# Performance work log

Measured on AMD Instinct MI355X. Metric: run time of the kernel, lower is better.

The kernel has to match this reference:

```python
import jax, jax.numpy as jnp
import numpy as np

N_EMBD = 768
N_HEAD = 12

def setup_inputs() -> dict:
    key = jax.random.key(0)
    ks = jax.random.split(key, 10)
    B, T, C = 2, 2048, N_EMBD
    s = 1.0 / np.sqrt(C)
    x = jax.random.normal(ks[0], (B, T, C), dtype=jnp.float32)
    attn_mask = jnp.ones((B, 1, T, T), dtype=jnp.float32)
    Wq = jax.random.normal(ks[1], (C, C), dtype=jnp.float32) * s
    bq = jax.random.normal(ks[2], (C,), dtype=jnp.float32) * 0.01
    Wk = jax.random.normal(ks[3], (C, C), dtype=jnp.float32) * s
    bk = jax.random.normal(ks[4], (C,), dtype=jnp.float32) * 0.01
    Wv = jax.random.normal(ks[5], (C, C), dtype=jnp.float32) * s
    bv = jax.random.normal(ks[6], (C,), dtype=jnp.float32) * 0.01
    Wp = jax.random.normal(ks[7], (C, C), dtype=jnp.float32) * s
    bp = jax.random.normal(ks[8], (C,), dtype=jnp.float32) * 0.01
    return {"x": x, "attn_mask": attn_mask, "Wq": Wq, "bq": bq, "Wk": Wk, "bk": bk,
            "Wv": Wv, "bv": bv, "Wp": Wp, "bp": bp}

def reference(x, attn_mask, Wq, bq, Wk, bk, Wv, bv, Wp, bp):
    B, T, C = x.shape
    H = N_HEAD
    hd = C // H
    # Linear layers (torch nn.Linear: y = x @ W.T + b)
    q = (x @ Wq.T + bq).reshape(B, T, H, hd).transpose(0, 2, 1, 3)  # [B,H,T,hd]
    k = (x @ Wk.T + bk).reshape(B, T, H, hd).transpose(0, 2, 1, 3)
    v = (x @ Wv.T + bv).reshape(B, T, H, hd).transpose(0, 2, 1, 3)
    att = jnp.einsum('bhqd,bhkd->bhqk', q, k) / jnp.sqrt(jnp.float32(hd))  # [B,H,T,T]
    causal = jnp.tril(jnp.ones((T, T), dtype=jnp.bool_))[None, None]       # [1,1,T,T]
    combined = causal & (attn_mask > 0)                                    # broadcast to [B,H,T,T]
    att = jnp.where(combined, att, -jnp.inf)
    att = jax.nn.softmax(att, axis=-1)
    y = jnp.einsum('bhqk,bhkd->bhqd', att, v)                              # [B,H,T,hd]
    y = y.transpose(0, 2, 1, 3).reshape(B, T, C)
    return y @ Wp.T + bp
```

## Files before the change

### kernel.cpp

```cpp
#include <hip/hip_runtime.h>
#include <hip/hip_bf16.h>
#include <cstdint>
#include <cstddef>

#define B_   2
#define H_   12
#define T_   2048
#define C_   768
#define HD_  64
#define M_   4096
#define NW_  (T_/64)
#define NPAIR 2

typedef __attribute__((ext_vector_type(8))) short bf16x8;
typedef __attribute__((ext_vector_type(4))) float fx4;
typedef __attribute__((ext_vector_type(16))) float f32x16;
typedef unsigned short u16;
typedef unsigned int   u32;
typedef unsigned long long u64;

static __device__ __forceinline__ u16 f2bf(float f){
    union { float f; unsigned int i; } c; c.f = f;
    unsigned int x = c.i;
    return (u16)((x + 0x7fffu + ((x >> 16) & 1u)) >> 16);
}

static __device__ __forceinline__ u32 pack_bf2(float a, float b){
    union { __hip_bfloat162 h; u32 u; } cv;
    cv.h = __float22bfloat162_rn(make_float2(a, b));
    return cv.u;
}

#define PREP_XBLK (M_ * C_ / 4 / 256)
#define PREP_WBLK (4 * C_ * C_ / 4 / 256)
#define PREP_MBLK (B_ * T_ * NW_ / 4)
__global__ void prep(const float* __restrict__ x,
                     const float* __restrict__ wq, const float* __restrict__ wk,
                     const float* __restrict__ wv, const float* __restrict__ wp,
                     const float* __restrict__ mask,
                     u16* __restrict__ xb, u16* __restrict__ wqkv, u64* __restrict__ bits)
{
    int bx = blockIdx.x;
    if (bx < PREP_XBLK){
        int i = bx * 256 + threadIdx.x;
        float4 v = ((const float4*)x)[i];
        ushort4 o;
        o.x = f2bf(v.x); o.y = f2bf(v.y); o.z = f2bf(v.z); o.w = f2bf(v.w);
        ((ushort4*)xb)[i] = o;
    } else if (bx < PREP_XBLK + PREP_WBLK){
        int i = (bx - PREP_XBLK) * 256 + threadIdx.x;
        int wsel = i / (C_ * C_ / 4);
        int wi   = i % (C_ * C_ / 4);
        const float* src = (wsel == 0) ? wq : (wsel == 1) ? wk : (wsel == 2) ? wv : wp;
        float4 v = ((const float4*)src)[wi];
        ushort4 o;
        o.x = f2bf(v.x); o.y = f2bf(v.y); o.z = f2bf(v.z); o.w = f2bf(v.w);
        ((ushort4*)wqkv)[i] = o;
    } else {
        int wid  = (bx - PREP_XBLK - PREP_WBLK) * 4 + (threadIdx.x >> 6);
        int lane = threadIdx.x & 63;
        float v = mask[(size_t)wid * 64 + lane];
        u64 m = __ballot(v > 0.0f);
        if (lane == 0) bits[wid] = m;
    }
}

__launch_bounds__(256, 2)
__global__ void gemm_qkv(const u16* __restrict__ xb, const u16* __restrict__ wqkv,
                         const float* __restrict__ bq, const float* __restrict__ bk,
                         const float* __restrict__ bv,
                         u16* __restrict__ qo, u16* __restrict__ ko, u16* __restrict__ vto)
{
    const int tid  = threadIdx.x;
    const int lane = tid & 63, wave = tid >> 6;
    const int l15 = lane & 15, lg = lane >> 4;
    int flat = blockIdx.x + 6 * (blockIdx.y + 32 * blockIdx.z);
    int swz  = (flat & 7) * 72 + (flat >> 3);
    const int n0 = (swz % 6) * 128;
    const int m0 = ((swz / 6) % 32) * 128;
    const int z  = swz / 192;
    const u16* wb     = wqkv + (size_t)z * C_ * C_;
    const float* bias = (z == 0) ? bq : (z == 1 ? bk : bv);
    const float oscl  = (z == 0) ? 0.1803368801111601f : 1.0f;

    __shared__ __align__(16) u16 lds_a[128 * 64];
    __shared__ __align__(16) u16 lds_b[128 * 64];

    fx4 acc[4][4];
    #pragma unroll
    for (int i = 0; i < 4; i++)
        #pragma unroll
        for (int j = 0; j < 4; j++) acc[i][j] = (fx4)0.0f;

    const int wm = (wave >> 1) * 64, wn = (wave & 1) * 64;
    const int sx = l15 & 7;

    for (int kt = 0; kt < C_ / 64; ++kt){
        const int k0 = kt * 64;
        #pragma unroll
        for (int c = 0; c < 4; ++c){
            int unit = c * 256 + tid;
            int row = unit >> 3, col = unit & 7;
            int gcol = (col ^ (row & 7)) * 8;
            const u16* ga = xb + (size_t)(m0 + row) * C_ + k0 + gcol;
            __builtin_amdgcn_global_load_lds((const __attribute__((address_space(1))) void*)ga,
                (__attribute__((address_space(3))) void*)(lds_a + (c * 256 + wave * 64) * 8), 16, 0, 0);
            const u16* gb = wb + (size_t)(n0 + row) * C_ + k0 + gcol;
            __builtin_amdgcn_global_load_lds((const __attribute__((address_space(1))) void*)gb,
                (__attribute__((address_space(3))) void*)(lds_b + (c * 256 + wave * 64) * 8), 16, 0, 0);
        }
        __syncthreads();
        #pragma unroll
        for (int ks = 0; ks < 2; ++ks){
            bf16x8 af[4], bfr[4];
            #pragma unroll
            for (int i = 0; i < 4; i++){
                af[i]  = *(const bf16x8*)&lds_a[(wm + i * 16 + l15) * 64 + (((4 * ks + lg) ^ sx) * 8)];
                bfr[i] = *(const bf16x8*)&lds_b[(wn + i * 16 + l15) * 64 + (((4 * ks + lg) ^ sx) * 8)];
            }
            #pragma unroll
            for (int i = 0; i < 4; i++)
                #pragma unroll
                for (int j = 0; j < 4; j++)
                    acc[i][j] = __builtin_amdgcn_mfma_f32_16x16x32_bf16(af[i], bfr[j], acc[i][j], 0, 0, 0);
        }
        __syncthreads();
    }

    #pragma unroll
    for (int i = 0; i < 4; i++){
        #pragma unroll
        for (int j = 0; j < 4; j++){
            #pragma unroll
            for (int r = 0; r < 4; r++){
                int m = m0 + wm + i * 16 + lg * 4 + r;
                int n = n0 + wn + j * 16 + l15;
                float v = (acc[i][j][r] + bias[n]) * oscl;
                u16 o = f2bf(v);
                int b = m >> 11, t = m & (T_ - 1);
                int h = n >> 6, d = n & 63;
                if (z == 2){
                    vto[(size_t)((b * H_ + h) * HD_ + d) * T_ + t] = o;
                } else {
                    u16* dst = (z == 0) ? qo : ko;
                    dst[(size_t)((b * H_ + h) * T_ + t) * HD_ + d] = o;
                }
            }
        }
    }
}

__launch_bounds__(256, 2)
__global__ void gemm_proj(const u16* __restrict__ yb, const u16* __restrict__ wp,
                          const float* __restrict__ bp, float* __restrict__ out)
{
    const int tid  = threadIdx.x;
    const int lane = tid & 63, wave = tid >> 6;
    const int l15 = lane & 15, lg = lane >> 4;
    int flat = blockIdx.x + 6 * blockIdx.y;
    int swz  = (flat & 7) * 24 + (flat >> 3);
    const int n0 = (swz % 6) * 128;
    const int m0 = (swz / 6) * 128;

    __shared__ __align__(16) u16 lds_a[128 * 64];
    __shared__ __align__(16) u16 lds_b[128 * 64];

    fx4 acc[4][4];
    #pragma unroll
    for (int i = 0; i < 4; i++)
        #pragma unroll
        for (int j = 0; j < 4; j++) acc[i][j] = (fx4)0.0f;

    const int wm = (wave >> 1) * 64, wn = (wave & 1) * 64;
    const int sx = l15 & 7;

    for (int kt = 0; kt < C_ / 64; ++kt){
        const int k0 = kt * 64;
        #pragma unroll
        for (int c = 0; c < 4; ++c){
            int unit = c * 256 + tid;
            int row = unit >> 3, col = unit & 7;
            int gcol = (col ^ (row & 7)) * 8;
            const u16* ga = yb + (size_t)(m0 + row) * C_ + k0 + gcol;
            __builtin_amdgcn_global_load_lds((const __attribute__((address_space(1))) void*)ga,
                (__attribute__((address_space(3))) void*)(lds_a + (c * 256 + wave * 64) * 8), 16, 0, 0);
            const u16* gb = wp + (size_t)(n0 + row) * C_ + k0 + gcol;
            __builtin_amdgcn_global_load_lds((const __attribute__((address_space(1))) void*)gb,
                (__attribute__((address_space(3))) void*)(lds_b + (c * 256 + wave * 64) * 8), 16, 0, 0);
        }
        __syncthreads();
        #pragma unroll
        for (int ks = 0; ks < 2; ++ks){
            bf16x8 af[4], bfr[4];
            #pragma unroll
            for (int i = 0; i < 4; i++){
                af[i]  = *(const bf16x8*)&lds_a[(wm + i * 16 + l15) * 64 + (((4 * ks + lg) ^ sx) * 8)];
                bfr[i] = *(const bf16x8*)&lds_b[(wn + i * 16 + l15) * 64 + (((4 * ks + lg) ^ sx) * 8)];
            }
            #pragma unroll
            for (int i = 0; i < 4; i++)
                #pragma unroll
                for (int j = 0; j < 4; j++)
                    acc[i][j] = __builtin_amdgcn_mfma_f32_16x16x32_bf16(af[i], bfr[j], acc[i][j], 0, 0, 0);
        }
        __syncthreads();
    }

    #pragma unroll
    for (int i = 0; i < 4; i++)
        #pragma unroll
        for (int j = 0; j < 4; j++)
            #pragma unroll
            for (int r = 0; r < 4; r++){
                int m = m0 + wm + i * 16 + lg * 4 + r;
                int n = n0 + wn + j * 16 + l15;
                out[(size_t)m * C_ + n] = acc[i][j][r] + bp[n];
            }
}

__launch_bounds__(256)
__global__ void attn(const u16* __restrict__ q, const u16* __restrict__ kmat,
                     const u16* __restrict__ vt, const u64* __restrict__ bits,
                     u16* __restrict__ y)
{
    const int tid = threadIdx.x;
    const int pr  = tid >> 7;
    const int ptid = tid & 127;
    const int w2  = (tid >> 6) & 1;
    const int lane = tid & 63;
    const int l31 = lane & 31, hi = lane >> 5;

    int flat = blockIdx.x;
    const int bh = (flat & 7) * 3 + ((flat >> 3) % 3);
    const int qt = 31 - (flat >> 3) / 3;
    const int b = bh / H_, h = bh % H_;
    const int qw0 = qt * 64 + 32 * w2;

    extern __shared__ __align__(16) u16 smem[];
    u16* lds_k = smem + (size_t)pr * 8192;
    u16* lds_v = lds_k + 4096;
    float* lds_ml = (float*)smem;

    const size_t bhoff = (size_t)bh * T_ * HD_;
    const u16* kb_ = kmat + bhoff;
    const u16* vb_ = vt + bhoff;

    bf16x8 qf[4];
    {
        const u16* qrow = q + bhoff + (size_t)(qw0 + l31) * HD_ + hi * 8;
        #pragma unroll
        for (int dc = 0; dc < 4; dc++)
            qf[dc] = *(const bf16x8*)(qrow + dc * 16);
    }

    f32x16 o0 = (f32x16)0.0f, o1 = (f32x16)0.0f;
    float m_l = -1e30f, l_l = 0.0f;

    const int nkt = qt + 1;
    const int nit = (nkt + NPAIR - 1) / NPAIR;
    const int qg  = qw0 + l31;
    const u64* brow = bits + (size_t)(b * T_ + qg) * NW_;

    for (int it = 0; it < nit; ++it){
        const int kt = it * NPAIR + pr;
        const bool valid = kt < nkt;
        const int kbase = kt * 64;

        if (it > 0) __syncthreads();
        if (valid){
            #pragma unroll
            for (int i = 0; i < 4; i++){
                int u = i * 128 + ptid;
                int row = u >> 3, col = u & 7;
                int gcol = (col ^ (row & 7)) * 8;
                __builtin_amdgcn_global_load_lds(
                    (const __attribute__((address_space(1))) void*)(kb_ + (size_t)(kbase + row) * HD_ + gcol),
                    (__attribute__((address_space(3))) void*)(lds_k + u * 8), 16, 0, 0);
                __builtin_amdgcn_global_load_lds(
                    (const __attribute__((address_space(1))) void*)(vb_ + (size_t)row * T_ + kbase + gcol),
                    (__attribute__((address_space(3))) void*)(lds_v + u * 8), 16, 0, 0);
            }
        }
        __syncthreads();

        if (valid){
            f32x16 s0 = (f32x16)0.0f, s1 = (f32x16)0.0f;
            #pragma unroll
            for (int dc = 0; dc < 4; dc++){
                bf16x8 kf0 = *(const bf16x8*)&lds_k[(l31     ) * 64 + (((2 * dc + hi) ^ (l31 & 7)) * 8)];
                bf16x8 kf1 = *(const bf16x8*)&lds_k[(l31 + 32) * 64 + (((2 * dc + hi) ^ (l31 & 7)) * 8)];
                s0 = __builtin_amdgcn_mfma_f32_32x32x16_bf16(kf0, qf[dc], s0, 0, 0, 0);
                s1 = __builtin_amdgcn_mfma_f32_32x32x16_bf16(kf1, qf[dc], s1, 0, 0, 0);
            }

            u64 raw = brow[kt];
            int sh = qg - kbase;
            u64 vis = sh < 0 ? 0ull : (sh >= 63 ? ~0ull : ((2ull << sh) - 1ull));
            u64 masked = raw & vis;
            if (!__all(masked == ~0ull)){
                u32 mk0 = (u32)(masked >> (4 * hi));
                u32 mk1 = (u32)(masked >> (32 + 4 * hi));
                #pragma unroll
                for (int r = 0; r < 16; r++){
                    int bpos = (r & 3) + 8 * (r >> 2);
                    s0[r] = ((mk0 >> bpos) & 1u) ? s0[r] : -1e30f;
                    s1[r] = ((mk1 >> bpos) & 1u) ? s1[r] : -1e30f;
                }
            }

            float mx = -1e30f;
            #pragma unroll
            for (int r = 0; r < 16; r++){ mx = fmaxf(mx, s0[r]); mx = fmaxf(mx, s1[r]); }
            mx = fmaxf(mx, __shfl_xor(mx, 32, 64));

            if (!__all(mx <= m_l + 10.0f)){
                float mnew = fmaxf(m_l, mx);
                float al = __builtin_amdgcn_exp2f(m_l - mnew);
                m_l = mnew;
                l_l *= al;
                #pragma unroll
                for (int r = 0; r < 16; r++){
                    int ql = (r & 3) + 8 * (r >> 2) + 4 * hi;
                    float a_r = __shfl(al, ql, 64);
                    o0[r] *= a_r; o1[r] *= a_r;
                }
            }

            float rs = 0.0f;
            bf16x8 pa[2][2];
            #pragma unroll
            for (int kb = 0; kb < 2; kb++){
                u32 P[8];
                #pragma unroll
                for (int g = 0; g < 8; g++){
                    float pe0 = __builtin_amdgcn_exp2f((kb ? s1[2*g]   : s0[2*g])   - m_l);
                    float pe1 = __builtin_amdgcn_exp2f((kb ? s1[2*g+1] : s0[2*g+1]) - m_l);
                    rs += pe0 + pe1;
                    P[g] = pack_bf2(pe0, pe1);
                }
                asm volatile("v_permlane32_swap_b32 %0, %1" : "+v"(P[0]), "+v"(P[2]));
                asm volatile("v_permlane32_swap_b32 %0, %1" : "+v"(P[1]), "+v"(P[3]));
                asm volatile("v_permlane32_swap_b32 %0, %1" : "+v"(P[4]), "+v"(P[6]));
                asm volatile("v_permlane32_swap_b32 %0, %1" : "+v"(P[5]), "+v"(P[7]));
                union { u32 uw[4]; bf16x8 v; } u0, u1;
                u0.uw[0]=P[0]; u0.uw[1]=P[1]; u0.uw[2]=P[2]; u0.uw[3]=P[3];
                u1.uw[0]=P[4]; u1.uw[1]=P[5]; u1.uw[2]=P[6]; u1.uw[3]=P[7];
                pa[kb][0] = u0.v; pa[kb][1] = u1.v;
            }
            rs += __shfl_xor(rs, 32, 64);
            l_l += rs;

            #pragma unroll
            for (int kb = 0; kb < 2; kb++)
                #pragma unroll
                for (int ks = 0; ks < 2; ks++){
                    int gidx = 4 * kb + 2 * ks + hi;
                    bf16x8 vf0 = *(const bf16x8*)&lds_v[(l31     ) * 64 + ((gidx ^ (l31 & 7)) * 8)];
                    bf16x8 vf1 = *(const bf16x8*)&lds_v[(l31 + 32) * 64 + ((gidx ^ (l31 & 7)) * 8)];
                    o0 = __builtin_amdgcn_mfma_f32_32x32x16_bf16(pa[kb][ks], vf0, o0, 0, 0, 0);
                    o1 = __builtin_amdgcn_mfma_f32_32x32x16_bf16(pa[kb][ks], vf1, o1, 0, 0, 0);
                }
        }
    }

    __syncthreads();
    {
        const int qrow = w2 * 32 + l31;
        if (hi == 0){
            lds_ml[(pr * 2 + 0) * 64 + qrow] = m_l;
            lds_ml[(pr * 2 + 1) * 64 + qrow] = l_l;
        }
        if (pr != 0){
            float* Od = (float*)(smem + (size_t)pr * 8192);
            #pragma unroll
            for (int r = 0; r < 16; r++){
                int ql = (r & 3) + 8 * (r >> 2) + 4 * hi;
                int row = w2 * 32 + ql;
                Od[row * 64 + l31]      = o0[r];
                Od[row * 64 + 32 + l31] = o1[r];
            }
        }
    }
    __syncthreads();

    if (pr == 0){
        const int qrow = w2 * 32 + l31;
        float mvals[NPAIR], lvals[NPAIR];
        mvals[0] = m_l; lvals[0] = l_l;
        #pragma unroll
        for (int p = 1; p < NPAIR; p++){
            mvals[p] = lds_ml[(p * 2 + 0) * 64 + qrow];
            lvals[p] = lds_ml[(p * 2 + 1) * 64 + qrow];
        }
        float mm = mvals[0];
        #pragma unroll
        for (int p = 1; p < NPAIR; p++) mm = fmaxf(mm, mvals[p]);
        float a[NPAIR], ltot = 0.0f;
        #pragma unroll
        for (int p = 0; p < NPAIR; p++){
            a[p] = __builtin_amdgcn_exp2f(mvals[p] - mm);
            ltot += lvals[p] * a[p];
        }
        float inv = 1.0f / ltot;

        #pragma unroll
        for (int r = 0; r < 16; r++){
            int ql = (r & 3) + 8 * (r >> 2) + 4 * hi;
            int row = w2 * 32 + ql;
            float a0r = __shfl(a[0], ql, 64);
            float v0 = o0[r] * a0r;
            float v1 = o1[r] * a0r;
            #pragma unroll
            for (int p = 1; p < NPAIR; p++){
                float apr = __shfl(a[p], ql, 64);
                const float* Od = (const float*)(smem + (size_t)p * 8192);
                v0 += Od[row * 64 + l31]      * apr;
                v1 += Od[row * 64 + 32 + l31] * apr;
            }
            float ivr = __shfl(inv, ql, 64);
            int trow = qt * 64 + row;
            u16* yr = y + (size_t)(b * T_ + trow) * C_ + h * HD_;
            yr[l31]      = f2bf(v0 * ivr);
            yr[32 + l31] = f2bf(v1 * ivr);
        }
    }
}

extern "C" void kernel_launch(void* const* d_in, const int* in_sizes, int n_in,
                              void* d_out, int out_size, void* d_ws, size_t ws_size,
                              hipStream_t stream)
{
    const float* x    = (const float*)d_in[0];
    const float* mask = (const float*)d_in[1];
    const float* Wq   = (const float*)d_in[2];
    const float* bq   = (const float*)d_in[3];
    const float* Wk   = (const float*)d_in[4];
    const float* bk   = (const float*)d_in[5];
    const float* Wv   = (const float*)d_in[6];
    const float* bv   = (const float*)d_in[7];
    const float* Wp   = (const float*)d_in[8];
    const float* bp   = (const float*)d_in[9];
    float* out = (float*)d_out;

    char* p = (char*)d_ws;
    u16* xb   = (u16*)p; p += (size_t)M_ * C_ * 2;
    u16* wqkv = (u16*)p; p += (size_t)4 * C_ * C_ * 2;
    u16* qo   = (u16*)p; p += (size_t)M_ * C_ * 2;
    u16* ko   = (u16*)p; p += (size_t)M_ * C_ * 2;
    u16* vto  = (u16*)p; p += (size_t)M_ * C_ * 2;
    u16* yb   = (u16*)p; p += (size_t)M_ * C_ * 2;
    u64* bits = (u64*)p; p += (size_t)B_ * T_ * NW_ * 8;

    prep<<<dim3(PREP_XBLK + PREP_WBLK + PREP_MBLK), 256, 0, stream>>>(
        x, Wq, Wk, Wv, Wp, mask, xb, wqkv, bits);

    gemm_qkv<<<dim3(C_ / 128, M_ / 128, 3), 256, 0, stream>>>(
        xb, wqkv, bq, bk, bv, qo, ko, vto);

    attn<<<dim3((T_ / 64) * B_ * H_), 256, NPAIR * 8192 * sizeof(u16), stream>>>(
        qo, ko, vto, bits, yb);

    gemm_proj<<<dim3(C_ / 128, M_ / 128), 256, 0, stream>>>(yb, wqkv + (size_t)3 * C_ * C_, bp, out);
}
```

Baseline: 113.8 us.

## Double-buffer LDS tiles in QKV and projection GEMMs to overlap loads with MFMA

Both GEMM kernels now use two LDS buffers per operand. The next K-tile is issued through global_load_lds into the alternate buffer while MFMAs run on the current one, so global-load latency overlaps with compute and one barrier per iteration is dropped. In exchange LDS use doubles to 64KB per block and the min-blocks-per-SM launch bound is removed, which can lower occupancy. The single barrier after compute must also cover completion of the async LDS writes, and the compiler's vmcnt handling decides whether real overlap happens.

```diff
diff --git a/kernel.cpp b/kernel.cpp
--- a/kernel.cpp
+++ b/kernel.cpp
@@ -65,7 +65,7 @@
     }
 }
 
-__launch_bounds__(256, 2)
+__launch_bounds__(256)
 __global__ void gemm_qkv(const u16* __restrict__ xb, const u16* __restrict__ wqkv,
                          const float* __restrict__ bq, const float* __restrict__ bk,
                          const float* __restrict__ bv,
@@ -83,8 +83,8 @@
     const float* bias = (z == 0) ? bq : (z == 1 ? bk : bv);
     const float oscl  = (z == 0) ? 0.1803368801111601f : 1.0f;
 
-    __shared__ __align__(16) u16 lds_a[128 * 64];
-    __shared__ __align__(16) u16 lds_b[128 * 64];
+    __shared__ __align__(16) u16 lds_a[2][128 * 64];
+    __shared__ __align__(16) u16 lds_b[2][128 * 64];
 
     fx4 acc[4][4];
     #pragma unroll
@@ -94,8 +94,9 @@
 
     const int wm = (wave >> 1) * 64, wn = (wave & 1) * 64;
     const int sx = l15 & 7;
-
-    for (int kt = 0; kt < C_ / 64; ++kt){
+    const int NT = C_ / 64;
+
+    auto stage = [&](int buf, int kt){
         const int k0 = kt * 64;
         #pragma unroll
         for (int c = 0; c < 4; ++c){
@@ -104,19 +105,25 @@
             int gcol = (col ^ (row & 7)) * 8;
             const u16* ga = xb + (size_t)(m0 + row) * C_ + k0 + gcol;
             __builtin_amdgcn_global_load_lds((const __attribute__((address_space(1))) void*)ga,
-                (__attribute__((address_space(3))) void*)(lds_a + (c * 256 + wave * 64) * 8), 16, 0, 0);
+                (__attribute__((address_space(3))) void*)(&lds_a[buf][(c * 256 + wave * 64) * 8]), 16, 0, 0);
             const u16* gb = wb + (size_t)(n0 + row) * C_ + k0 + gcol;
             __builtin_amdgcn_global_load_lds((const __attribute__((address_space(1))) void*)gb,
-                (__attribute__((address_space(3))) void*)(lds_b + (c * 256 + wave * 64) * 8), 16, 0, 0);
-        }
-        __syncthreads();
+                (__attribute__((address_space(3))) void*)(&lds_b[buf][(c * 256 + wave * 64) * 8]), 16, 0, 0);
+        }
+    };
+
+    stage(0, 0);
+    __syncthreads();
+    int cur = 0;
+    for (int kt = 0; kt < NT; ++kt){
+        if (kt + 1 < NT) stage(cur ^ 1, kt + 1);
         #pragma unroll
         for (int ks = 0; ks < 2; ++ks){
             bf16x8 af[4], bfr[4];
             #pragma unroll
             for (int i = 0; i < 4; i++){
-                af[i]  = *(const bf16x8*)&lds_a[(wm + i * 16 + l15) * 64 + (((4 * ks + lg) ^ sx) * 8)];
-                bfr[i] = *(const bf16x8*)&lds_b[(wn + i * 16 + l15) * 64 + (((4 * ks + lg) ^ sx) * 8)];
+                af[i]  = *(const bf16x8*)&lds_a[cur][(wm + i * 16 + l15) * 64 + (((4 * ks + lg) ^ sx) * 8)];
+                bfr[i] = *(const bf16x8*)&lds_b[cur][(wn + i * 16 + l15) * 64 + (((4 * ks + lg) ^ sx) * 8)];
             }
             #pragma unroll
             for (int i = 0; i < 4; i++)
@@ -125,6 +132,7 @@
                     acc[i][j] = __builtin_amdgcn_mfma_f32_16x16x32_bf16(af[i], bfr[j], acc[i][j], 0, 0, 0);
         }
         __syncthreads();
+        cur ^= 1;
     }
 
     #pragma unroll
@@ -150,7 +158,7 @@
     }
 }
 
-__launch_bounds__(256, 2)
+__launch_bounds__(256)
 __global__ void gemm_proj(const u16* __restrict__ yb, const u16* __restrict__ wp,
                           const float* __restrict__ bp, float* __restrict__ out)
 {
@@ -162,8 +170,8 @@
     const int n0 = (swz % 6) * 128;
     const int m0 = (swz / 6) * 128;
 
-    __shared__ __align__(16) u16 lds_a[128 * 64];
-    __shared__ __align__(16) u16 lds_b[128 * 64];
+    __shared__ __align__(16) u16 lds_a[2][128 * 64];
+    __shared__ __align__(16) u16 lds_b[2][128 * 64];
 
     fx4 acc[4][4];
     #pragma unroll
@@ -173,8 +181,9 @@
 
     const int wm = (wave >> 1) * 64, wn = (wave & 1) * 64;
     const int sx = l15 & 7;
-
-    for (int kt = 0; kt < C_ / 64; ++kt){
+    const int NT = C_ / 64;
+
+    auto stage = [&](int buf, int kt){
         const int k0 = kt * 64;
         #pragma unroll
         for (int c = 0; c < 4; ++c){
@@ -183,19 +192,25 @@
             int gcol = (col ^ (row & 7)) * 8;
             const u16* ga = yb + (size_t)(m0 + row) * C_ + k0 + gcol;
             __builtin_amdgcn_global_load_lds((const __attribute__((address_space(1))) void*)ga,
-                (__attribute__((address_space(3))) void*)(lds_a + (c * 256 + wave * 64) * 8), 16, 0, 0);
+                (__attribute__((address_space(3))) void*)(&lds_a[buf][(c * 256 + wave * 64) * 8]), 16, 0, 0);
             const u16* gb = wp + (size_t)(n0 + row) * C_ + k0 + gcol;
             __builtin_amdgcn_global_load_lds((const __attribute__((address_space(1))) void*)gb,
-                (__attribute__((address_space(3))) void*)(lds_b + (c * 256 + wave * 64) * 8), 16, 0, 0);
-        }
-        __syncthreads();
+                (__attribute__((address_space(3))) void*)(&lds_b[buf][(c * 256 + wave * 64) * 8]), 16, 0, 0);
+        }
+    };
+
+    stage(0, 0);
+    __syncthreads();
+    int cur = 0;
+    for (int kt = 0; kt < NT; ++kt){
+        if (kt + 1 < NT) stage(cur ^ 1, kt + 1);
         #pragma unroll
         for (int ks = 0; ks < 2; ++ks){
             bf16x8 af[4], bfr[4];
             #pragma unroll
             for (int i = 0; i < 4; i++){
-                af[i]  = *(const bf16x8*)&lds_a[(wm + i * 16 + l15) * 64 + (((4 * ks + lg) ^ sx) * 8)];
-                bfr[i] = *(const bf16x8*)&lds_b[(wn + i * 16 + l15) * 64 + (((4 * ks + lg) ^ sx) * 8)];
+                af[i]  = *(const bf16x8*)&lds_a[cur][(wm + i * 16 + l15) * 64 + (((4 * ks + lg) ^ sx) * 8)];
+                bfr[i] = *(const bf16x8*)&lds_b[cur][(wn + i * 16 + l15) * 64 + (((4 * ks + lg) ^ sx) * 8)];
             }
             #pragma unroll
             for (int i = 0; i < 4; i++)
@@ -204,6 +219,7 @@
                     acc[i][j] = __builtin_amdgcn_mfma_f32_16x16x32_bf16(af[i], bfr[j], acc[i][j], 0, 0, 0);
         }
         __syncthreads();
+        cur ^= 1;
     }
 
     #pragma unroll
```

Result: no change. 115.2 us (+1.2%).
